# Performance work log

Hardware: AMD Instinct MI355X
Metric: run time of the kernel (lower is better)

## Reference

```python
import jax, jax.numpy as jnp
import numpy as np

ND, NT, E, B = 10000, 10000, 500000, 8192
DF, TF, H, CF, P1, P2 = 256, 256, 128, 954, 2048, 512
NEG_SLOPE = 0.2


def _gat(xs, Ws, a_s, xd, Wd, a_d, b, src, dst, n_dst):
    # PyG GATConv (heads=1, add_self_loops=False): gather -> edge softmax -> scatter-sum
    hs = xs @ Ws                    # [Ns, H] transformed source features
    hd = xd @ Wd                    # [Nd, H] transformed destination features
    es = hs @ a_s                   # [Ns] per-src attention logits
    ed = hd @ a_d                   # [Nd] per-dst attention logits
    e = jax.nn.leaky_relu(es[src] + ed[dst], NEG_SLOPE)          # [E]
    m = jax.ops.segment_max(e, dst, num_segments=n_dst)
    ex = jnp.exp(e - m[dst])
    den = jax.ops.segment_sum(ex, dst, num_segments=n_dst)
    alpha = ex / (den[dst] + 1e-16)                              # edge softmax per dst
    out = jax.ops.segment_sum(alpha[:, None] * hs[src], dst, num_segments=n_dst)
    return out + b


def _reduction(x, W1, b1, W2, b2, W3, b3):
    # F.normalize(x, 2, 1) then Linear/ReLU x3 (dropout is identity in eval)
    nrm = jnp.maximum(jnp.linalg.norm(x, axis=1, keepdims=True), 1e-12)
    x = x / nrm
    x = jax.nn.relu(x @ W1 + b1)
    x = jax.nn.relu(x @ W2 + b2)
    return jax.nn.relu(x @ W3 + b3)


def setup_inputs() -> dict:
    key = jax.random.key(0)
    ks = iter(jax.random.split(key, 64))
    def n(shape, s=0.05):
        return jax.random.normal(next(ks), shape, dtype=jnp.float32) * s
    def ri(maxv, shape):
        return jax.random.randint(next(ks), shape, 0, maxv, dtype=jnp.int32)
    return {
        'x_drug': n((ND, DF), 1.0), 'x_target': n((NT, TF), 1.0),
        'cell_features': n((B, CF), 1.0),
        'dd_W': n((DF, H)), 'dd_as': n((H,)), 'dd_ad': n((H,)), 'dd_b': n((H,)),
        'dt_Ws': n((DF, H)), 'dt_Wd': n((TF, H)), 'dt_as': n((H,)), 'dt_ad': n((H,)), 'dt_b': n((H,)),
        'td_Ws': n((TF, H)), 'td_Wd': n((DF, H)), 'td_as': n((H,)), 'td_ad': n((H,)), 'td_b': n((H,)),
        'tt_W': n((TF, H)), 'tt_as': n((H,)), 'tt_ad': n((H,)), 'tt_b': n((H,)),
        'r1_W1': n((CF, P1)), 'r1_b1': n((P1,)), 'r1_W2': n((P1, P2)), 'r1_b2': n((P2,)), 'r1_W3': n((P2, 2 * H)), 'r1_b3': n((2 * H,)),
        'r2_W1': n((4 * H, P1)), 'r2_b1': n((P1,)), 'r2_W2': n((P1, P2)), 'r2_b2': n((P2,)), 'r2_W3': n((P2, H)), 'r2_b3': n((H,)),
        'cls_W': n((H, 2)), 'cls_b': n((2,)),
        'e_dd_src': ri(ND, (E,)), 'e_dd_dst': ri(ND, (E,)),
        'e_dt_src': ri(ND, (E,)), 'e_dt_dst': ri(NT, (E,)),
        'e_td_src': ri(NT, (E,)), 'e_td_dst': ri(ND, (E,)),
        'e_tt_src': ri(NT, (E,)), 'e_tt_dst': ri(NT, (E,)),
        'drug1_id': ri(ND, (B,)), 'drug2_id': ri(ND, (B,)),
    }


def reference(x_drug, x_target, cell_features,
              dd_W, dd_as, dd_ad, dd_b,
              dt_Ws, dt_Wd, dt_as, dt_ad, dt_b,
              td_Ws, td_Wd, td_as, td_ad, td_b,
              tt_W, tt_as, tt_ad, tt_b,
              r1_W1, r1_b1, r1_W2, r1_b2, r1_W3, r1_b3,
              r2_W1, r2_b1, r2_W2, r2_b2, r2_W3, r2_b3,
              cls_W, cls_b,
              e_dd_src, e_dd_dst, e_dt_src, e_dt_dst,
              e_td_src, e_td_dst, e_tt_src, e_tt_dst,
              drug1_id, drug2_id):
    # HeteroConv with aggr='sum': drug <- (d-d) + (rev_d-t); target <- (d-t) + (t-t); then relu
    drug_out = jax.nn.relu(
        _gat(x_drug, dd_W, dd_as, x_drug, dd_W, dd_ad, dd_b, e_dd_src, e_dd_dst, ND)
        + _gat(x_target, td_Ws, td_as, x_drug, td_Wd, td_ad, td_b, e_td_src, e_td_dst, ND))
    target_out = jax.nn.relu(
        _gat(x_drug, dt_Ws, dt_as, x_target, dt_Wd, dt_ad, dt_b, e_dt_src, e_dt_dst, NT)
        + _gat(x_target, tt_W, tt_as, x_target, tt_W, tt_ad, tt_b, e_tt_src, e_tt_dst, NT))
    cell = _reduction(cell_features, r1_W1, r1_b1, r1_W2, r1_b2, r1_W3, r1_b3)   # [B, 2H]
    hidden = jnp.concatenate([drug_out[drug1_id], drug_out[drug2_id], cell], axis=1)  # [B, 4H]
    hidden = _reduction(hidden, r2_W1, r2_b1, r2_W2, r2_b2, r2_W3, r2_b3)        # [B, H]
    logits = hidden @ cls_W + cls_b                                              # [B, 2]
    return (logits, drug_out, target_out)
```

## Files before the change

### kernel.cpp

```cpp
#include <hip/hip_runtime.h>

#define ND 10000
#define NT_ 10000
#define EE 500000
#define BB 8192
#define DF 256
#define TFD 256
#define HH 128
#define CF 954
#define CFP 960
#define P1C 2048
#define P2C 512
#define MPAD 10112

#define CHUNK 4096
#define NCH 123
#define NBK 157
#define MAXB 6144
#define GCAP 256

typedef unsigned short u16;
typedef __attribute__((ext_vector_type(8))) short short8;
typedef __attribute__((ext_vector_type(4))) float f4;

#define AS1 __attribute__((address_space(1)))
#define AS3 __attribute__((address_space(3)))
#define GLOAD16(g, l) \
  __builtin_amdgcn_global_load_lds((const AS1 void*)(g), (AS3 void*)(l), 16, 0, 0)

__device__ inline u16 f2bf(float f) {
  unsigned int u = __builtin_bit_cast(unsigned int, f);
  unsigned int r = (u + 0x7FFFu + ((u >> 16) & 1u)) >> 16;
  return (u16)r;
}
__device__ inline float bf2f(u16 b) {
  return __builtin_bit_cast(float, ((unsigned int)b) << 16);
}
__device__ inline float ldval(float v) { return v; }
__device__ inline float ldval(u16 v) { return bf2f(v); }

__device__ inline void load8cvt(const float* p, u16* dst) {
#pragma unroll
  for (int i = 0; i < 4; ++i) {
    float2 v = reinterpret_cast<const float2*>(p)[i];
    dst[2 * i] = f2bf(v.x);
    dst[2 * i + 1] = f2bf(v.y);
  }
}

__device__ inline int xcd_swz(int bid, int nwg) {
  return ((nwg & 7) == 0) ? ((bid & 7) * (nwg >> 3) + (bid >> 3)) : bid;
}

__global__ void __launch_bounds__(256) xcvt_kernel(const float* __restrict__ xd,
                                                   const float* __restrict__ xt,
                                                   u16* __restrict__ xdb,
                                                   u16* __restrict__ xtb) {
  const float* X = blockIdx.y ? xt : xd;
  u16* Y = blockIdx.y ? xtb : xdb;
  long i = (long)blockIdx.x * 256 + threadIdx.x;
  long e = i * 8;
  int row = (int)(e >> 8);
  union { u16 u[8]; short8 v; } tv;
  if (row < ND) {
    load8cvt(X + e, tv.u);
  } else {
#pragma unroll
    for (int k = 0; k < 8; ++k) tv.u[k] = 0;
  }
  *reinterpret_cast<short8*>(Y + e) = tv.v;
}

struct TransArgs {
  const float* W[12];
  u16* Wt[12];
  int K[12];
  int N[12];
  int Kp[12];
};

__global__ void __launch_bounds__(256) transpose_all(TransArgs ta) {
  const int id = blockIdx.y;
  const int K = ta.K[id], N = ta.N[id], Kp = ta.Kp[id];
  const int tn = (N + 31) >> 5, tk = (Kp + 31) >> 5;
  if ((int)blockIdx.x >= tn * tk) return;
  const float* W = ta.W[id];
  u16* Wt = ta.Wt[id];
  const int bn = (blockIdx.x % tn) << 5;
  const int bk = (blockIdx.x / tn) << 5;
  __shared__ u16 tile[32][33];
  const int tx = threadIdx.x;
  const int ty = threadIdx.y;
#pragma unroll
  for (int i = ty; i < 32; i += 8) {
    int k = bk + i, n = bn + tx;
    tile[i][tx] = (k < K && n < N) ? f2bf(W[(long)k * N + n]) : (u16)0;
  }
  __syncthreads();
#pragma unroll
  for (int i = ty; i < 32; i += 8) {
    int n = bn + i, k = bk + tx;
    if (n < N && k < Kp) Wt[(long)n * Kp + k] = tile[tx][i];
  }
}

template <int ACT, int BIAS, int RSCALE>
__global__ void __launch_bounds__(256) gemm_db(const u16* __restrict__ A,
                                               const u16* __restrict__ Bt,
                                               const float* __restrict__ bias,
                                               const float* __restrict__ rs,
                                               u16* __restrict__ C, int M, int N, int K) {
  const int bid = xcd_swz(blockIdx.x, gridDim.x);
  const int tiles_n = N >> 7;
  const int bm = bid / tiles_n;
  const int bn = bid % tiles_n;
  const long row0 = (long)bm << 7;
  const int col0 = bn << 7;
  __shared__ u16 sh[16384];
  const int t = threadIdx.x;
  const int lane = t & 63;
  const int w = t >> 6;
  const int wr = w >> 1, wc = w & 1;
  const int lr = lane & 15, lk = lane >> 4;
  const int srow = lane >> 2;
  const int scol = (lane & 3) << 3;
  const u16* gA0 = A + (row0 + (w << 4) + srow) * K + scol;
  const u16* gA1 = A + (row0 + ((w + 4) << 4) + srow) * K + scol;
  const u16* gB0 = Bt + ((long)col0 + (w << 4) + srow) * K + scol;
  const u16* gB1 = Bt + ((long)col0 + ((w + 4) << 4) + srow) * K + scol;
  const int lofs0 = (w << 4) * 32;
  const int lofs1 = ((w + 4) << 4) * 32;
  f4 acc[4][4] = {};
  const int nk = K >> 5;

#define STAGE4(kt_, b_)                                     \
  do {                                                      \
    const int ko = (kt_) << 5;                              \
    u16* ab = sh + (b_) * 8192;                             \
    u16* bb = ab + 4096;                                    \
    GLOAD16(gA0 + ko, ab + lofs0);                          \
    GLOAD16(gA1 + ko, ab + lofs1);                          \
    GLOAD16(gB0 + ko, bb + lofs0);                          \
    GLOAD16(gB1 + ko, bb + lofs1);                          \
  } while (0)

  STAGE4(0, 0);
  __syncthreads();
  int cur = 0;
  for (int kt = 0; kt < nk; ++kt) {
    if (kt + 1 < nk) STAGE4(kt + 1, cur ^ 1);
    const u16* Ab = sh + cur * 8192;
    const u16* Bb = Ab + 4096;
    short8 af[4], bf[4];
#pragma unroll
    for (int m = 0; m < 4; ++m)
      af[m] = *reinterpret_cast<const short8*>(&Ab[(((wr << 6) + (m << 4) + lr) << 5) + (lk << 3)]);
#pragma unroll
    for (int n = 0; n < 4; ++n)
      bf[n] = *reinterpret_cast<const short8*>(&Bb[(((wc << 6) + (n << 4) + lr) << 5) + (lk << 3)]);
#pragma unroll
    for (int m = 0; m < 4; ++m)
#pragma unroll
      for (int n = 0; n < 4; ++n)
        acc[m][n] = __builtin_amdgcn_mfma_f32_16x16x32_bf16(af[m], bf[n], acc[m][n], 0, 0, 0);
    __syncthreads();
    cur ^= 1;
  }
#undef STAGE4

  float bv[4];
#pragma unroll
  for (int n = 0; n < 4; ++n)
    bv[n] = BIAS ? bias[col0 + (wc << 6) + (n << 4) + lr] : 0.0f;
#pragma unroll
  for (int m = 0; m < 4; ++m) {
#pragma unroll
    for (int r = 0; r < 4; ++r) {
      const int row = (wr << 6) + (m << 4) + (lk << 2) + r;
      const float rsv = RSCALE ? rs[row0 + row] : 1.0f;
#pragma unroll
      for (int n = 0; n < 4; ++n) {
        const int col = (wc << 6) + (n << 4) + lr;
        float x = acc[m][n][r];
        if (RSCALE) x *= rsv;
        x += bv[n];
        if (ACT) x = fmaxf(x, 0.0f);
        sh[(row << 7) + col] = f2bf(x);
      }
    }
  }
  __syncthreads();
#pragma unroll
  for (int i = 0; i < 8; ++i) {
    const int c = t + (i << 8);
    const int rr = c >> 4, off = (c & 15) << 3;
    *reinterpret_cast<short8*>(&C[(row0 + rr) * N + col0 + off]) =
        *reinterpret_cast<const short8*>(&sh[(rr << 7) + off]);
  }
}

template <int ACT, int BIAS>
__global__ void __launch_bounds__(256) gemm_db64(const u16* __restrict__ A,
                                                 const u16* __restrict__ Bt,
                                                 const float* __restrict__ bias,
                                                 u16* __restrict__ C, int M, int N, int K) {
  const int bid = xcd_swz(blockIdx.x, gridDim.x);
  const int tiles_n = N >> 7;
  const int bm = bid / tiles_n;
  const int bn = bid % tiles_n;
  const long row0 = (long)bm << 6;
  const int col0 = bn << 7;
  __shared__ u16 sh[12288];
  const int t = threadIdx.x;
  const int lane = t & 63;
  const int w = t >> 6;
  const int wr = w >> 1, wc = w & 1;
  const int lr = lane & 15, lk = lane >> 4;
  const int srow = lane >> 2;
  const int scol = (lane & 3) << 3;
  const u16* gA0 = A + (row0 + (w << 4) + srow) * K + scol;
  const u16* gB0 = Bt + ((long)col0 + (w << 4) + srow) * K + scol;
  const u16* gB1 = Bt + ((long)col0 + ((w + 4) << 4) + srow) * K + scol;
  const int lofs0 = (w << 4) * 32;
  const int lofs1 = ((w + 4) << 4) * 32;
  f4 acc[2][4] = {};
  const int nk = K >> 5;

#define STAGE3(kt_, b_)                                     \
  do {                                                      \
    const int ko = (kt_) << 5;                              \
    u16* ab = sh + (b_) * 6144;                             \
    u16* bb = ab + 2048;                                    \
    GLOAD16(gA0 + ko, ab + lofs0);                          \
    GLOAD16(gB0 + ko, bb + lofs0);                          \
    GLOAD16(gB1 + ko, bb + lofs1);                          \
  } while (0)

  STAGE3(0, 0);
  __syncthreads();
  int cur = 0;
  for (int kt = 0; kt < nk; ++kt) {
    if (kt + 1 < nk) STAGE3(kt + 1, cur ^ 1);
    const u16* Ab = sh + cur * 6144;
    const u16* Bb = Ab + 2048;
    short8 af[2], bf[4];
#pragma unroll
    for (int m = 0; m < 2; ++m)
      af[m] = *reinterpret_cast<const short8*>(&Ab[(((wr << 5) + (m << 4) + lr) << 5) + (lk << 3)]);
#pragma unroll
    for (int n = 0; n < 4; ++n)
      bf[n] = *reinterpret_cast<const short8*>(&Bb[(((wc << 6) + (n << 4) + lr) << 5) + (lk << 3)]);
#pragma unroll
    for (int m = 0; m < 2; ++m)
#pragma unroll
      for (int n = 0; n < 4; ++n)
        acc[m][n] = __builtin_amdgcn_mfma_f32_16x16x32_bf16(af[m], bf[n], acc[m][n], 0, 0, 0);
    __syncthreads();
    cur ^= 1;
  }
#undef STAGE3

  float bv[4];
#pragma unroll
  for (int n = 0; n < 4; ++n)
    bv[n] = BIAS ? bias[col0 + (wc << 6) + (n << 4) + lr] : 0.0f;
#pragma unroll
  for (int m = 0; m < 2; ++m) {
#pragma unroll
    for (int n = 0; n < 4; ++n) {
      const int col = (wc << 6) + (n << 4) + lr;
#pragma unroll
      for (int r = 0; r < 4; ++r) {
        const int row = (wr << 5) + (m << 4) + (lk << 2) + r;
        float x = acc[m][n][r] + bv[n];
        if (ACT) x = fmaxf(x, 0.0f);
        sh[(row << 7) + col] = f2bf(x);
      }
    }
  }
  __syncthreads();
#pragma unroll
  for (int i = 0; i < 4; ++i) {
    const int c = t + (i << 8);
    const int rr = c >> 4, off = (c & 15) << 3;
    *reinterpret_cast<short8*>(&C[(row0 + rr) * N + col0 + off]) =
        *reinterpret_cast<const short8*>(&sh[(rr << 7) + off]);
  }
}

struct NodeEd {
  const float* a0[3];
  const float* a1[3];
  float* e0[3];
  float* e1[3];
};

__global__ void __launch_bounds__(256) gemm_node(const u16* __restrict__ A,
                                                 const u16* __restrict__ Bt,
                                                 u16* __restrict__ C, NodeEd ne) {
  const int M = MPAD, N = 384, K = 256;
  const int bid = blockIdx.x;
  const int tiles_n = 3;
  const int bm = bid / tiles_n;
  const int bn = bid % tiles_n;
  const long row0 = (long)bm << 6;
  const int col0 = bn << 7;
  __shared__ u16 sh[12288];
  const int t = threadIdx.x;
  const int lane = t & 63;
  const int w = t >> 6;
  const int wr = w >> 1, wc = w & 1;
  const int lr = lane & 15, lk = lane >> 4;
  const int srow = lane >> 2;
  const int scol = (lane & 3) << 3;
  const u16* gA0 = A + (row0 + (w << 4) + srow) * K + scol;
  const u16* gB0 = Bt + ((long)col0 + (w << 4) + srow) * K + scol;
  const u16* gB1 = Bt + ((long)col0 + ((w + 4) << 4) + srow) * K + scol;
  const int lofs0 = (w << 4) * 32;
  const int lofs1 = ((w + 4) << 4) * 32;
  f4 acc[2][4] = {};
  const int nk = K >> 5;

#define STAGE3(kt_, b_)                                     \
  do {                                                      \
    const int ko = (kt_) << 5;                              \
    u16* ab = sh + (b_) * 6144;                             \
    u16* bb = ab + 2048;                                    \
    GLOAD16(gA0 + ko, ab + lofs0);                          \
    GLOAD16(gB0 + ko, bb + lofs0);                          \
    GLOAD16(gB1 + ko, bb + lofs1);                          \
  } while (0)

  STAGE3(0, 0);
  __syncthreads();
  int cur = 0;
  for (int kt = 0; kt < nk; ++kt) {
    if (kt + 1 < nk) STAGE3(kt + 1, cur ^ 1);
    const u16* Ab = sh + cur * 6144;
    const u16* Bb = Ab + 2048;
    short8 af[2], bf[4];
#pragma unroll
    for (int m = 0; m < 2; ++m)
      af[m] = *reinterpret_cast<const short8*>(&Ab[(((wr << 5) + (m << 4) + lr) << 5) + (lk << 3)]);
#pragma unroll
    for (int n = 0; n < 4; ++n)
      bf[n] = *reinterpret_cast<const short8*>(&Bb[(((wc << 6) + (n << 4) + lr) << 5) + (lk << 3)]);
#pragma unroll
    for (int m = 0; m < 2; ++m)
#pragma unroll
      for (int n = 0; n < 4; ++n)
        acc[m][n] = __builtin_amdgcn_mfma_f32_16x16x32_bf16(af[m], bf[n], acc[m][n], 0, 0, 0);
    __syncthreads();
    cur ^= 1;
  }
#undef STAGE3

#pragma unroll
  for (int m = 0; m < 2; ++m) {
#pragma unroll
    for (int n = 0; n < 4; ++n) {
      const int col = (wc << 6) + (n << 4) + lr;
#pragma unroll
      for (int r = 0; r < 4; ++r) {
        const int row = (wr << 5) + (m << 4) + (lk << 2) + r;
        sh[(row << 7) + col] = f2bf(acc[m][n][r]);
      }
    }
  }
  __syncthreads();
#pragma unroll
  for (int i = 0; i < 4; ++i) {
    const int c = t + (i << 8);
    const int rr = c >> 4, off = (c & 15) << 3;
    *reinterpret_cast<short8*>(&C[(row0 + rr) * N + col0 + off]) =
        *reinterpret_cast<const short8*>(&sh[(rr << 7) + off]);
  }
  const float* a0 = ne.a0[bn];
  const float* a1 = ne.a1[bn];
  if (a0 || a1) {
    const int r = t >> 2, qq = t & 3;
    const u16* hrow = sh + (r << 7) + (qq << 5);
    float p0 = 0.f, p1 = 0.f;
#pragma unroll
    for (int c = 0; c < 32; ++c) {
      float hv = bf2f(hrow[c]);
      if (a0) p0 += hv * a0[(qq << 5) + c];
      if (a1) p1 += hv * a1[(qq << 5) + c];
    }
    p0 += __shfl_xor(p0, 1); p0 += __shfl_xor(p0, 2);
    p1 += __shfl_xor(p1, 1); p1 += __shfl_xor(p1, 2);
    const int grow = (int)row0 + r;
    if (qq == 0 && grow < ND) {
      if (ne.e0[bn]) ne.e0[bn][grow] = p0;
      if (ne.e1[bn]) ne.e1[bn][grow] = p1;
    }
  }
}

struct EdgePtrs {
  const int* dst[4];
  const int* src[4];
};

__global__ void __launch_bounds__(256) sort_count(EdgePtrs ep, int* __restrict__ hist) {
  const int cv = blockIdx.y, ch = blockIdx.x;
  __shared__ int h[NBK];
  for (int i = threadIdx.x; i < NBK; i += 256) h[i] = 0;
  __syncthreads();
  const int* dst = ep.dst[cv];
  const int e0 = ch * CHUNK;
  const int e1 = e0 + CHUNK < EE ? e0 + CHUNK : EE;
  for (int i = e0 + threadIdx.x; i < e1; i += 256) atomicAdd(&h[dst[i] >> 6], 1);
  __syncthreads();
  int* out = hist + ((long)cv * NCH + ch) * NBK;
  for (int i = threadIdx.x; i < NBK; i += 256) out[i] = h[i];
}

__global__ void __launch_bounds__(256) sort_scan(int* __restrict__ hist, int* __restrict__ base,
                                                 int* __restrict__ offs_all) {
  const int cv = blockIdx.x;
  int* H = hist + (long)cv * NCH * NBK;
  __shared__ int tot[NBK];
  for (int b = threadIdx.x; b < NBK; b += 256) {
    int run = 0;
    for (int ch = 0; ch < NCH; ++ch) {
      int v = H[ch * NBK + b];
      H[ch * NBK + b] = run;
      run += v;
    }
    tot[b] = run;
  }
  __syncthreads();
  if (threadIdx.x == 0) {
    int* B = base + cv * (NBK + 1);
    int run = 0;
    for (int b = 0; b < NBK; ++b) { B[b] = run; run += tot[b]; }
    B[NBK] = run;
    offs_all[(long)cv * 10001 + 10000] = run;
  }
}

__global__ void __launch_bounds__(256) sort_scatter(EdgePtrs ep, const int* __restrict__ hist,
                                                    const int* __restrict__ base,
                                                    unsigned int* __restrict__ binned) {
  const int cv = blockIdx.y, ch = blockIdx.x;
  __shared__ int lcnt[NBK];
  __shared__ int lofs[NBK];
  __shared__ int lcur[NBK];
  __shared__ int sofs[NBK];
  __shared__ unsigned int buf[CHUNK];
  for (int i = threadIdx.x; i < NBK; i += 256) lcnt[i] = 0;
  __syncthreads();
  const int* dst = ep.dst[cv];
  const int* src = ep.src[cv];
  const int e0 = ch * CHUNK;
  const int e1 = e0 + CHUNK < EE ? e0 + CHUNK : EE;
  const int n = e1 - e0;
  unsigned int pk[16];
#pragma unroll
  for (int u = 0; u < 16; ++u) {
    int i = e0 + u * 256 + threadIdx.x;
    unsigned int p = 0xFFFFFFFFu;
    if (i < e1) {
      int d = dst[i];
      p = ((unsigned int)d << 16) | (unsigned int)src[i];
      atomicAdd(&lcnt[d >> 6], 1);
    }
    pk[u] = p;
  }
  {
    const int* chOfs = hist + ((long)cv * NCH + ch) * NBK;
    const int* B = base + cv * (NBK + 1);
    for (int b = threadIdx.x; b < NBK; b += 256) sofs[b] = B[b] + chOfs[b];
  }
  __syncthreads();
  if (threadIdx.x == 0) {
    int run = 0;
    for (int b = 0; b < NBK; ++b) { lofs[b] = run; lcur[b] = run; run += lcnt[b]; }
  }
  __syncthreads();
#pragma unroll
  for (int u = 0; u < 16; ++u) {
    if (pk[u] != 0xFFFFFFFFu) {
      int b = pk[u] >> 22;
      int p = atomicAdd(&lcur[b], 1);
      buf[p] = pk[u];
    }
  }
  __syncthreads();
  unsigned int* outp = binned + (long)cv * EE;
  for (int i = threadIdx.x; i < n; i += 256) {
    unsigned int p = buf[i];
    int b = p >> 22;
    outp[sofs[b] + (i - lofs[b])] = p;
  }
}

__global__ void __launch_bounds__(256) sort_bucket(const unsigned int* __restrict__ binned,
                                                   const int* __restrict__ base,
                                                   int* __restrict__ offs_all,
                                                   u16* __restrict__ srcs) {
  const int cv = blockIdx.y, b = blockIdx.x;
  const int* B = base + cv * (NBK + 1);
  const int s0 = B[b], s1 = B[b + 1];
  int n = s1 - s0;
  if (n > MAXB) n = MAXB;
  __shared__ unsigned int buf[MAXB];
  __shared__ u16 obuf[MAXB];
  __shared__ int cnt[64], dofs[64], dcur[64];
  if (threadIdx.x < 64) cnt[threadIdx.x] = 0;
  __syncthreads();
  const unsigned int* inp = binned + (long)cv * EE + s0;
  for (int i = threadIdx.x; i < n; i += 256) {
    unsigned int p = inp[i];
    buf[i] = p;
    atomicAdd(&cnt[(p >> 16) & 63], 1);
  }
  __syncthreads();
  if (threadIdx.x == 0) {
    int run = 0;
    for (int i = 0; i < 64; ++i) { dofs[i] = run; dcur[i] = run; run += cnt[i]; }
  }
  __syncthreads();
  if (threadIdx.x < 64) {
    int d = (b << 6) + threadIdx.x;
    if (d < 10000) offs_all[(long)cv * 10001 + d] = s0 + dofs[threadIdx.x];
  }
  for (int i = threadIdx.x; i < n; i += 256) {
    unsigned int p = buf[i];
    int pos = atomicAdd(&dcur[(p >> 16) & 63], 1);
    obuf[pos] = (u16)(p & 0xFFFFu);
  }
  __syncthreads();
  u16* outp = srcs + (long)cv * EE + s0;
  for (int i = threadIdx.x; i < n; i += 256) outp[i] = obuf[i];
}

struct GatArgs {
  const int* offs[4];
  const u16* srcs[4];
  const float* es[4];
  const float* ed[4];
  const u16* hs[4];
  const float* bias[4];
};

__global__ void __launch_bounds__(256) gat3(GatArgs ga, float* __restrict__ out,
                                            u16* __restrict__ feat) {
  const int t = threadIdx.x;
  const int w = t >> 6;
  const int lane = t & 63;
  const int hi = lane >> 5;
  const int fl = (lane & 31) << 2;
  const int d = blockIdx.x * 4 + w;
  const int half = blockIdx.y;
  __shared__ float al[4][GCAP + 2];
  __shared__ u16 sl[4][GCAP + 2];
  float a0 = 0.f, a1 = 0.f, a2 = 0.f, a3 = 0.f;
#pragma unroll
  for (int q = 0; q < 2; ++q) {
    const int cv = half * 2 + q;
    const int* offs = ga.offs[cv];
    const int o0 = offs[d], o1 = offs[d + 1];
    const int deg = o1 - o0;
    const u16* sp = ga.srcs[cv] + o0;
    const float* es = ga.es[cv];
    const float edd = ga.ed[cv][d];
    const u16* hs = ga.hs[cv];
    const int degc = deg > GCAP ? GCAP : deg;
    __syncthreads();
    float part = 0.f;
    for (int j = lane; j < degc; j += 64) {
      int s = sp[j];
      float e = es[s] + edd;
      e = e > 0.f ? e : 0.2f * e;
      float ex = __expf(e);
      al[w][j] = ex;
      sl[w][j] = (u16)s;
      part += ex;
    }
    for (int j = GCAP + lane; j < deg; j += 64) {
      float e = es[sp[j]] + edd;
      e = e > 0.f ? e : 0.2f * e;
      part += __expf(e);
    }
#pragma unroll
    for (int o = 32; o > 0; o >>= 1) part += __shfl_down(part, o);
    const float inv = 1.0f / (__shfl(part, 0) + 1e-16f);
    for (int j = lane; j < degc; j += 64) al[w][j] *= inv;
    if (lane == 0 && (degc & 1)) { al[w][degc] = 0.f; sl[w][degc] = 0; }
    __syncthreads();
    const int npair = (degc + 1) >> 1;
#pragma unroll 4
    for (int k = 0; k < npair; ++k) {
      const int j = 2 * k + hi;
      const float wgt = al[w][j];
      const int s = sl[w][j];
      ushort4 v = *reinterpret_cast<const ushort4*>(hs + (long)s * 384 + fl);
      a0 += wgt * bf2f(v.x);
      a1 += wgt * bf2f(v.y);
      a2 += wgt * bf2f(v.z);
      a3 += wgt * bf2f(v.w);
    }
    if (hi == 0) {
      for (int j = GCAP; j < deg; ++j) {
        int s = sp[j];
        float e = es[s] + edd;
        e = e > 0.f ? e : 0.2f * e;
        float wgt = __expf(e) * inv;
        ushort4 v = *reinterpret_cast<const ushort4*>(hs + (long)s * 384 + fl);
        a0 += wgt * bf2f(v.x); a1 += wgt * bf2f(v.y);
        a2 += wgt * bf2f(v.z); a3 += wgt * bf2f(v.w);
      }
    }
  }
  a0 += __shfl_xor(a0, 32);
  a1 += __shfl_xor(a1, 32);
  a2 += __shfl_xor(a2, 32);
  a3 += __shfl_xor(a3, 32);
  if (hi == 0) {
    const float* b1 = ga.bias[half * 2];
    const float* b2 = ga.bias[half * 2 + 1];
    float4 bb1 = *reinterpret_cast<const float4*>(b1 + fl);
    float4 bb2 = *reinterpret_cast<const float4*>(b2 + fl);
    float4 r;
    r.x = fmaxf(a0 + bb1.x + bb2.x, 0.0f);
    r.y = fmaxf(a1 + bb1.y + bb2.y, 0.0f);
    r.z = fmaxf(a2 + bb1.z + bb2.z, 0.0f);
    r.w = fmaxf(a3 + bb1.w + bb2.w, 0.0f);
    *reinterpret_cast<float4*>(out + 16384 + (long)half * ND * HH + (long)d * HH + fl) = r;
    if (half == 0) {
      ushort4 fv;
      fv.x = f2bf(r.x); fv.y = f2bf(r.y); fv.z = f2bf(r.z); fv.w = f2bf(r.w);
      *reinterpret_cast<ushort4*>(feat + (long)d * HH + fl) = fv;
    }
  }
}

template <typename T>
__global__ void __launch_bounds__(256) rownorm_kernel(const T* __restrict__ X,
                                                      u16* __restrict__ Y, int Kin, int Kout) {
  const int row = blockIdx.x;
  const int t = threadIdx.x;
  const T* xr = X + (long)row * Kin;
  float ss = 0.f;
  for (int k = t; k < Kin; k += 256) {
    float v = ldval(xr[k]);
    ss += v * v;
  }
#pragma unroll
  for (int o = 32; o > 0; o >>= 1) ss += __shfl_down(ss, o);
  __shared__ float sh[4];
  if ((t & 63) == 0) sh[t >> 6] = ss;
  __syncthreads();
  float tot = sh[0] + sh[1] + sh[2] + sh[3];
  float inv = 1.0f / fmaxf(sqrtf(tot), 1e-12f);
  u16* yr = Y + (long)row * Kout;
  for (int k = t; k < Kin; k += 256) yr[k] = f2bf(ldval(xr[k]) * inv);
  for (int k = Kin + t; k < Kout; k += 256) yr[k] = 0;
}

__global__ void __launch_bounds__(256) buildprep_kernel(const u16* __restrict__ feat,
                                                        const int* __restrict__ id1,
                                                        const int* __restrict__ id2,
                                                        const u16* __restrict__ cell,
                                                        u16* __restrict__ hidraw,
                                                        float* __restrict__ hinvn) {
  const int row = blockIdx.x;
  const int t = threadIdx.x;
  const int i1 = id1[row], i2 = id2[row];
  u16 v[2];
  float ss = 0.f;
#pragma unroll
  for (int u = 0; u < 2; ++u) {
    const int col = t + (u << 8);
    u16 x;
    if (col < 128) x = feat[(long)i1 * HH + col];
    else if (col < 256) x = feat[(long)i2 * HH + (col - 128)];
    else x = cell[(long)row * 256 + (col - 256)];
    v[u] = x;
    float f = bf2f(x);
    ss += f * f;
  }
#pragma unroll
  for (int o = 32; o > 0; o >>= 1) ss += __shfl_down(ss, o);
  __shared__ float sh[4];
  if ((t & 63) == 0) sh[t >> 6] = ss;
  __syncthreads();
  const float tot = sh[0] + sh[1] + sh[2] + sh[3];
  hidraw[(long)row * 512 + t] = v[0];
  hidraw[(long)row * 512 + t + 256] = v[1];
  if (t == 0) hinvn[row] = 1.0f / fmaxf(sqrtf(tot), 1e-12f);
}

__global__ void __launch_bounds__(128) logits_kernel(const u16* __restrict__ h2,
                                                     const float* __restrict__ W,
                                                     const float* __restrict__ b,
                                                     float* __restrict__ out) {
  const int row = blockIdx.x;
  const int t = threadIdx.x;
  float hv = bf2f(h2[(long)row * HH + t]);
  float p0 = hv * W[2 * t], p1 = hv * W[2 * t + 1];
#pragma unroll
  for (int o = 32; o > 0; o >>= 1) {
    p0 += __shfl_down(p0, o);
    p1 += __shfl_down(p1, o);
  }
  __shared__ float sA[2], sB[2];
  if ((t & 63) == 0) { sA[t >> 6] = p0; sB[t >> 6] = p1; }
  __syncthreads();
  if (t == 0) {
    out[2 * row] = sA[0] + sA[1] + b[0];
    out[2 * row + 1] = sB[0] + sB[1] + b[1];
  }
}

extern "C" void kernel_launch(void* const* d_in, const int* in_sizes, int n_in,
                              void* d_out, int out_size, void* d_ws, size_t ws_size,
                              hipStream_t stream) {
  const float* x_drug = (const float*)d_in[0];
  const float* x_target = (const float*)d_in[1];
  const float* cellf = (const float*)d_in[2];
  const float* dd_W = (const float*)d_in[3];
  const float* dd_as = (const float*)d_in[4];
  const float* dd_ad = (const float*)d_in[5];
  const float* dd_b = (const float*)d_in[6];
  const float* dt_Ws = (const float*)d_in[7];
  const float* dt_Wd = (const float*)d_in[8];
  const float* dt_as = (const float*)d_in[9];
  const float* dt_ad = (const float*)d_in[10];
  const float* dt_b = (const float*)d_in[11];
  const float* td_Ws = (const float*)d_in[12];
  const float* td_Wd = (const float*)d_in[13];
  const float* td_as = (const float*)d_in[14];
  const float* td_ad = (const float*)d_in[15];
  const float* td_b = (const float*)d_in[16];
  const float* tt_W = (const float*)d_in[17];
  const float* tt_as = (const float*)d_in[18];
  const float* tt_ad = (const float*)d_in[19];
  const float* tt_b = (const float*)d_in[20];
  const float* r1_W1 = (const float*)d_in[21];
  const float* r1_b1 = (const float*)d_in[22];
  const float* r1_W2 = (const float*)d_in[23];
  const float* r1_b2 = (const float*)d_in[24];
  const float* r1_W3 = (const float*)d_in[25];
  const float* r1_b3 = (const float*)d_in[26];
  const float* r2_W1 = (const float*)d_in[27];
  const float* r2_b1 = (const float*)d_in[28];
  const float* r2_W2 = (const float*)d_in[29];
  const float* r2_b2 = (const float*)d_in[30];
  const float* r2_W3 = (const float*)d_in[31];
  const float* r2_b3 = (const float*)d_in[32];
  const float* cls_W = (const float*)d_in[33];
  const float* cls_b = (const float*)d_in[34];
  const int* src_dd = (const int*)d_in[35];
  const int* dst_dd = (const int*)d_in[36];
  const int* src_dt = (const int*)d_in[37];
  const int* dst_dt = (const int*)d_in[38];
  const int* src_td = (const int*)d_in[39];
  const int* dst_td = (const int*)d_in[40];
  const int* src_tt = (const int*)d_in[41];
  const int* dst_tt = (const int*)d_in[42];
  const int* drug1 = (const int*)d_in[43];
  const int* drug2 = (const int*)d_in[44];
  float* out = (float*)d_out;

  char* ws = (char*)d_ws;
  size_t cur = 0;
  auto alloc = [&](size_t b) {
    size_t r = cur;
    cur += (b + 255) & ~(size_t)255;
    return r;
  };

  u16* xdb = (u16*)(ws + alloc((size_t)MPAD * DF * 2));
  u16* xtb = (u16*)(ws + alloc((size_t)MPAD * TFD * 2));
  u16* Bd = (u16*)(ws + alloc((size_t)384 * DF * 2));
  u16* Bt6 = (u16*)(ws + alloc((size_t)384 * TFD * 2));
  u16* wt1 = (u16*)(ws + alloc((size_t)P1C * CFP * 2));
  u16* wt2 = (u16*)(ws + alloc((size_t)P2C * P1C * 2));
  u16* wt3 = (u16*)(ws + alloc((size_t)256 * P2C * 2));
  u16* wt4 = (u16*)(ws + alloc((size_t)P1C * 512 * 2));
  u16* wt5 = (u16*)(ws + alloc((size_t)P2C * P1C * 2));
  u16* wt6 = (u16*)(ws + alloc((size_t)HH * P2C * 2));
  u16* h6d = (u16*)(ws + alloc((size_t)MPAD * 384 * 2));
  u16* h6t = (u16*)(ws + alloc((size_t)MPAD * 384 * 2));
  float* es0 = (float*)(ws + alloc(ND * 4));
  float* ed0 = (float*)(ws + alloc(ND * 4));
  float* es1 = (float*)(ws + alloc(NT_ * 4));
  float* ed1 = (float*)(ws + alloc(ND * 4));
  float* es2 = (float*)(ws + alloc(ND * 4));
  float* ed2 = (float*)(ws + alloc(NT_ * 4));
  float* es3 = (float*)(ws + alloc(NT_ * 4));
  float* ed3 = (float*)(ws + alloc(NT_ * 4));
  int* hist = (int*)(ws + alloc((size_t)4 * NCH * NBK * 4));
  int* base = (int*)(ws + alloc((size_t)4 * (NBK + 1) * 4));
  int* offs_all = (int*)(ws + alloc((size_t)4 * 10001 * 4));
  unsigned int* binned = (unsigned int*)(ws + alloc((size_t)4 * EE * 4));
  u16* srcs = (u16*)(ws + alloc((size_t)4 * EE * 2));
  u16* feat = (u16*)(ws + alloc((size_t)ND * HH * 2));
  u16* cellnorm = (u16*)(ws + alloc((size_t)BB * CFP * 2));
  u16* big = (u16*)(ws + alloc((size_t)BB * P1C * 2));
  u16* mid = (u16*)(ws + alloc((size_t)BB * P2C * 2));
  u16* cellout = (u16*)(ws + alloc((size_t)BB * 256 * 2));
  u16* hidraw = (u16*)(ws + alloc((size_t)BB * 512 * 2));
  float* hinvn = (float*)(ws + alloc((size_t)BB * 4));
  u16* h2 = (u16*)(ws + alloc((size_t)BB * HH * 2));

  xcvt_kernel<<<dim3(MPAD * DF / 8 / 256, 2), 256, 0, stream>>>(x_drug, x_target, xdb, xtb);

  TransArgs ta;
  const float* tw[12] = {dd_W, td_Wd, dt_Ws, td_Ws, dt_Wd, tt_W, r1_W1, r1_W2, r1_W3, r2_W1, r2_W2, r2_W3};
  u16* twt[12] = {Bd, Bd + 128 * 256, Bd + 2 * 128 * 256, Bt6, Bt6 + 128 * 256, Bt6 + 2 * 128 * 256,
                  wt1, wt2, wt3, wt4, wt5, wt6};
  int tk_[12] = {DF, DF, DF, TFD, TFD, TFD, CF, P1C, P2C, 512, P1C, P2C};
  int tn_[12] = {HH, HH, HH, HH, HH, HH, P1C, P2C, 256, P1C, P2C, HH};
  int tp_[12] = {DF, DF, DF, TFD, TFD, TFD, CFP, P1C, P2C, 512, P1C, P2C};
  for (int i = 0; i < 12; ++i) {
    ta.W[i] = tw[i]; ta.Wt[i] = twt[i]; ta.K[i] = tk_[i]; ta.N[i] = tn_[i]; ta.Kp[i] = tp_[i];
  }
  transpose_all<<<dim3(1920, 12), dim3(32, 8), 0, stream>>>(ta);

  const u16* h_dd = h6d;
  const u16* h_tdd = h6d + 128;
  const u16* h_dts = h6d + 256;
  const u16* h_tds = h6t;
  const u16* h_dtd = h6t + 128;
  const u16* h_tt = h6t + 256;

  NodeEd ndd;
  ndd.a0[0] = dd_as; ndd.a1[0] = dd_ad; ndd.e0[0] = es0; ndd.e1[0] = ed0;
  ndd.a0[1] = nullptr; ndd.a1[1] = td_ad; ndd.e0[1] = nullptr; ndd.e1[1] = ed1;
  ndd.a0[2] = dt_as; ndd.a1[2] = nullptr; ndd.e0[2] = es2; ndd.e1[2] = nullptr;
  gemm_node<<<(MPAD / 64) * 3, 256, 0, stream>>>(xdb, Bd, h6d, ndd);
  NodeEd ntt;
  ntt.a0[0] = td_as; ntt.a1[0] = nullptr; ntt.e0[0] = es1; ntt.e1[0] = nullptr;
  ntt.a0[1] = nullptr; ntt.a1[1] = dt_ad; ntt.e0[1] = nullptr; ntt.e1[1] = ed2;
  ntt.a0[2] = tt_as; ntt.a1[2] = tt_ad; ntt.e0[2] = es3; ntt.e1[2] = ed3;
  gemm_node<<<(MPAD / 64) * 3, 256, 0, stream>>>(xtb, Bt6, h6t, ntt);

  EdgePtrs ep;
  ep.dst[0] = dst_dd; ep.dst[1] = dst_td; ep.dst[2] = dst_dt; ep.dst[3] = dst_tt;
  ep.src[0] = src_dd; ep.src[1] = src_td; ep.src[2] = src_dt; ep.src[3] = src_tt;
  sort_count<<<dim3(NCH, 4), 256, 0, stream>>>(ep, hist);
  sort_scan<<<4, 256, 0, stream>>>(hist, base, offs_all);
  sort_scatter<<<dim3(NCH, 4), 256, 0, stream>>>(ep, hist, base, binned);
  sort_bucket<<<dim3(NBK, 4), 256, 0, stream>>>(binned, base, offs_all, srcs);

  GatArgs gaa;
  float* ees[4] = {es0, es1, es2, es3};
  float* eed[4] = {ed0, ed1, ed2, ed3};
  const u16* ghs[4] = {h_dd, h_tds, h_dts, h_tt};
  const float* gbias[4] = {dd_b, td_b, dt_b, tt_b};
  for (int i = 0; i < 4; ++i) {
    gaa.offs[i] = offs_all + (long)i * 10001;
    gaa.srcs[i] = srcs + (long)i * EE;
    gaa.es[i] = ees[i];
    gaa.ed[i] = eed[i];
    gaa.hs[i] = ghs[i];
    gaa.bias[i] = gbias[i];
  }
  gat3<<<dim3(2500, 2), 256, 0, stream>>>(gaa, out, feat);

  rownorm_kernel<float><<<BB, 256, 0, stream>>>(cellf, cellnorm, CF, CFP);
  gemm_db<1, 1, 0><<<(BB / 128) * (P1C / 128), 256, 0, stream>>>(cellnorm, wt1, r1_b1, nullptr,
                                                                 big, BB, P1C, CFP);
  gemm_db64<1, 1><<<(BB / 64) * (P2C / 128), 256, 0, stream>>>(big, wt2, r1_b2, mid, BB, P2C, P1C);
  gemm_db64<1, 1><<<(BB / 64) * (256 / 128), 256, 0, stream>>>(mid, wt3, r1_b3, cellout, BB, 256, P2C);
  buildprep_kernel<<<BB, 256, 0, stream>>>(feat, drug1, drug2, cellout, hidraw, hinvn);
  gemm_db<1, 1, 1><<<(BB / 128) * (P1C / 128), 256, 0, stream>>>(hidraw, wt4, r2_b1, hinvn,
                                                                 big, BB, P1C, 512);
  gemm_db64<1, 1><<<(BB / 64) * (P2C / 128), 256, 0, stream>>>(big, wt5, r2_b2, mid, BB, P2C, P1C);
  gemm_db64<1, 1><<<(BB / 64) * (HH / 128), 256, 0, stream>>>(mid, wt6, r2_b3, h2, BB, HH, P2C);
  logits_kernel<<<BB, 128, 0, stream>>>(h2, cls_W, cls_b, out);
}
```

Before: 317.2 us.

## Split GAT aggregation per relation into separate blocks with a combine kernel

The GAT kernel now launches one block per relation and destination group, 10000 blocks instead of 5000, each handling a single edge type rather than looping over two. Per-relation partial sums are written to a new float workspace. A separate combine kernel then adds bias, sums the relation pairs, applies ReLU and writes the bf16 features. Softmax normalisation is now applied to the accumulators once, instead of rescaling every shared-memory weight. The change aims for more parallelism and shorter per-block critical paths, at the cost of an extra 20 MB write/read round trip and one more kernel launch.

```diff
diff --git a/kernel.cpp b/kernel.cpp
--- a/kernel.cpp
+++ b/kernel.cpp
@@ -542,76 +542,71 @@
   const float* es[4];
   const float* ed[4];
   const u16* hs[4];
-  const float* bias[4];
 };
 
-__global__ void __launch_bounds__(256) gat3(GatArgs ga, float* __restrict__ out,
-                                            u16* __restrict__ feat) {
+__global__ void __launch_bounds__(256) gat5(GatArgs ga, float* __restrict__ part) {
   const int t = threadIdx.x;
   const int w = t >> 6;
   const int lane = t & 63;
   const int hi = lane >> 5;
   const int fl = (lane & 31) << 2;
-  const int d = blockIdx.x * 4 + w;
-  const int half = blockIdx.y;
+  const int b = blockIdx.x;
+  const int cv = (b & 7) >> 1;
+  const int j = ((b >> 3) << 1) | (b & 1);
+  const int d = j * 4 + w;
   __shared__ float al[4][GCAP + 2];
   __shared__ u16 sl[4][GCAP + 2];
   float a0 = 0.f, a1 = 0.f, a2 = 0.f, a3 = 0.f;
-#pragma unroll
-  for (int q = 0; q < 2; ++q) {
-    const int cv = half * 2 + q;
-    const int* offs = ga.offs[cv];
-    const int o0 = offs[d], o1 = offs[d + 1];
-    const int deg = o1 - o0;
-    const u16* sp = ga.srcs[cv] + o0;
-    const float* es = ga.es[cv];
-    const float edd = ga.ed[cv][d];
-    const u16* hs = ga.hs[cv];
-    const int degc = deg > GCAP ? GCAP : deg;
-    __syncthreads();
-    float part = 0.f;
-    for (int j = lane; j < degc; j += 64) {
-      int s = sp[j];
+  const int* offs = ga.offs[cv];
+  const int o0 = offs[d], o1 = offs[d + 1];
+  const int deg = o1 - o0;
+  const u16* sp = ga.srcs[cv] + o0;
+  const float* es = ga.es[cv];
+  const float edd = ga.ed[cv][d];
+  const u16* hs = ga.hs[cv];
+  const int degc = deg > GCAP ? GCAP : deg;
+  float part1 = 0.f;
+  for (int jj = lane; jj < degc; jj += 64) {
+    int s = sp[jj];
+    float e = es[s] + edd;
+    e = e > 0.f ? e : 0.2f * e;
+    float ex = __expf(e);
+    al[w][jj] = ex;
+    sl[w][jj] = (u16)s;
+    part1 += ex;
+  }
+  for (int jj = GCAP + lane; jj < deg; jj += 64) {
+    float e = es[sp[jj]] + edd;
+    e = e > 0.f ? e : 0.2f * e;
+    part1 += __expf(e);
+  }
+#pragma unroll
+  for (int o = 32; o > 0; o >>= 1) part1 += __shfl_down(part1, o);
+  const float inv = 1.0f / (__shfl(part1, 0) + 1e-16f);
+  if (lane == 0 && (degc & 1)) { al[w][degc] = 0.f; sl[w][degc] = 0; }
+  __syncthreads();
+  const int npair = (degc + 1) >> 1;
+#pragma unroll 4
+  for (int k = 0; k < npair; ++k) {
+    const int jj = 2 * k + hi;
+    const float wgt = al[w][jj];
+    const int s = sl[w][jj];
+    ushort4 v = *reinterpret_cast<const ushort4*>(hs + (long)s * 384 + fl);
+    a0 += wgt * bf2f(v.x);
+    a1 += wgt * bf2f(v.y);
+    a2 += wgt * bf2f(v.z);
+    a3 += wgt * bf2f(v.w);
+  }
+  a0 *= inv; a1 *= inv; a2 *= inv; a3 *= inv;
+  if (hi == 0) {
+    for (int jj = GCAP; jj < deg; ++jj) {
+      int s = sp[jj];
       float e = es[s] + edd;
       e = e > 0.f ? e : 0.2f * e;
-      float ex = __expf(e);
-      al[w][j] = ex;
-      sl[w][j] = (u16)s;
-      part += ex;
-    }
-    for (int j = GCAP + lane; j < deg; j += 64) {
-      float e = es[sp[j]] + edd;
-      e = e > 0.f ? e : 0.2f * e;
-      part += __expf(e);
-    }
-#pragma unroll
-    for (int o = 32; o > 0; o >>= 1) part += __shfl_down(part, o);
-    const float inv = 1.0f / (__shfl(part, 0) + 1e-16f);
-    for (int j = lane; j < degc; j += 64) al[w][j] *= inv;
-    if (lane == 0 && (degc & 1)) { al[w][degc] = 0.f; sl[w][degc] = 0; }
-    __syncthreads();
-    const int npair = (degc + 1) >> 1;
-#pragma unroll 4
-    for (int k = 0; k < npair; ++k) {
-      const int j = 2 * k + hi;
-      const float wgt = al[w][j];
-      const int s = sl[w][j];
+      float wgt = __expf(e) * inv;
       ushort4 v = *reinterpret_cast<const ushort4*>(hs + (long)s * 384 + fl);
-      a0 += wgt * bf2f(v.x);
-      a1 += wgt * bf2f(v.y);
-      a2 += wgt * bf2f(v.z);
-      a3 += wgt * bf2f(v.w);
-    }
-    if (hi == 0) {
-      for (int j = GCAP; j < deg; ++j) {
-        int s = sp[j];
-        float e = es[s] + edd;
-        e = e > 0.f ? e : 0.2f * e;
-        float wgt = __expf(e) * inv;
-        ushort4 v = *reinterpret_cast<const ushort4*>(hs + (long)s * 384 + fl);
-        a0 += wgt * bf2f(v.x); a1 += wgt * bf2f(v.y);
-        a2 += wgt * bf2f(v.z); a3 += wgt * bf2f(v.w);
-      }
+      a0 += wgt * bf2f(v.x); a1 += wgt * bf2f(v.y);
+      a2 += wgt * bf2f(v.z); a3 += wgt * bf2f(v.w);
     }
   }
   a0 += __shfl_xor(a0, 32);
@@ -619,22 +614,27 @@
   a2 += __shfl_xor(a2, 32);
   a3 += __shfl_xor(a3, 32);
   if (hi == 0) {
-    const float* b1 = ga.bias[half * 2];
-    const float* b2 = ga.bias[half * 2 + 1];
-    float4 bb1 = *reinterpret_cast<const float4*>(b1 + fl);
-    float4 bb2 = *reinterpret_cast<const float4*>(b2 + fl);
     float4 r;
-    r.x = fmaxf(a0 + bb1.x + bb2.x, 0.0f);
-    r.y = fmaxf(a1 + bb1.y + bb2.y, 0.0f);
-    r.z = fmaxf(a2 + bb1.z + bb2.z, 0.0f);
-    r.w = fmaxf(a3 + bb1.w + bb2.w, 0.0f);
-    *reinterpret_cast<float4*>(out + 16384 + (long)half * ND * HH + (long)d * HH + fl) = r;
-    if (half == 0) {
-      ushort4 fv;
-      fv.x = f2bf(r.x); fv.y = f2bf(r.y); fv.z = f2bf(r.z); fv.w = f2bf(r.w);
-      *reinterpret_cast<ushort4*>(feat + (long)d * HH + fl) = fv;
-    }
-  }
+    r.x = a0; r.y = a1; r.z = a2; r.w = a3;
+    *reinterpret_cast<float4*>(part + ((long)cv * ND + d) * HH + fl) = r;
+  }
+}
+
+__global__ void __launch_bounds__(256) gat_combine(const float* __restrict__ part,
+                                                   const float* __restrict__ b0,
+                                                   const float* __restrict__ b1,
+                                                   const float* __restrict__ b2,
+                                                   const float* __restrict__ b3,
+                                                   float* __restrict__ out,
+                                                   u16* __restrict__ feat) {
+  const int half = blockIdx.y;
+  const long i = (long)blockIdx.x * 256 + threadIdx.x;
+  const int h = (int)(i & (HH - 1));
+  float v = part[(long)(half * 2) * ND * HH + i] + part[(long)(half * 2 + 1) * ND * HH + i];
+  v += half ? (b2[h] + b3[h]) : (b0[h] + b1[h]);
+  v = fmaxf(v, 0.0f);
+  out[16384 + (long)half * ND * HH + i] = v;
+  if (half == 0) feat[i] = f2bf(v);
 }
 
 template <typename T>
@@ -798,6 +798,7 @@
   int* offs_all = (int*)(ws + alloc((size_t)4 * 10001 * 4));
   unsigned int* binned = (unsigned int*)(ws + alloc((size_t)4 * EE * 4));
   u16* srcs = (u16*)(ws + alloc((size_t)4 * EE * 2));
+  float* part = (float*)(ws + alloc((size_t)4 * ND * HH * 4));
   u16* feat = (u16*)(ws + alloc((size_t)ND * HH * 2));
   u16* cellnorm = (u16*)(ws + alloc((size_t)BB * CFP * 2));
   u16* big = (u16*)(ws + alloc((size_t)BB * P1C * 2));
@@ -851,16 +852,15 @@
   float* ees[4] = {es0, es1, es2, es3};
   float* eed[4] = {ed0, ed1, ed2, ed3};
   const u16* ghs[4] = {h_dd, h_tds, h_dts, h_tt};
-  const float* gbias[4] = {dd_b, td_b, dt_b, tt_b};
   for (int i = 0; i < 4; ++i) {
     gaa.offs[i] = offs_all + (long)i * 10001;
     gaa.srcs[i] = srcs + (long)i * EE;
     gaa.es[i] = ees[i];
     gaa.ed[i] = eed[i];
     gaa.hs[i] = ghs[i];
-    gaa.bias[i] = gbias[i];
-  }
-  gat3<<<dim3(2500, 2), 256, 0, stream>>>(gaa, out, feat);
+  }
+  gat5<<<10000, 256, 0, stream>>>(gaa, part);
+  gat_combine<<<dim3(ND * HH / 256, 2), 256, 0, stream>>>(part, dd_b, td_b, dt_b, tt_b, out, feat);
 
   rownorm_kernel<float><<<BB, 256, 0, stream>>>(cellf, cellnorm, CF, CFP);
   gemm_db<1, 1, 0><<<(BB / 128) * (P1C / 128), 256, 0, stream>>>(cellnorm, wt1, r1_b1, nullptr,
```

New measurement: 325.7 us. +2.7%, slower.
